# Optimization experiments

Measured on AMD Instinct MI355X. Metric: run time of the kernel, lower is better.

## Reference

```python
import jax, jax.numpy as jnp
import numpy as np

B, N, E = 4, 160, 200000
D_EDGE, D_ORI, D_TYPE = 128, 8, 120      # d_edge, d_ori_edge, d_edge_type = d_edge - d_ori_edge
D_EXT = 512                               # d_edge * expansion_factor(4)
D_H4 = 512                                # d_edge * 4
D_REL = 16
PML, ETN = 32, 16                         # path_max_length, edge_type_num


def setup_inputs() -> dict:
    key = jax.random.key(0)
    ks = jax.random.split(key, 16)
    p = lambda i, shape, s=0.05: (jax.random.normal(ks[i], shape) * s).astype(jnp.float32)
    return dict(
        rel_type=jax.random.randint(ks[0], (E,), 0, ETN),
        rel_error=jax.random.normal(ks[1], (E, D_ORI), jnp.float32),
        edge_pos=jax.random.randint(ks[2], (E,), 0, PML),
        dist=jax.random.randint(ks[3], (B, N, N), 0, PML),
        rel_row=jnp.sort(jax.random.randint(ks[4], (E,), 0, B * N * N)),
        rel_col=jax.random.randint(ks[5], (E,), 0, 10000),
        batch_num=B, max_node=N,
        type_tab=p(6, (ETN, D_TYPE), 1.0),
        pos_tab=p(7, (PML, D_EDGE), 1.0),
        dist_tab=p(8, (PML, D_EXT), 1.0),
        w1=p(9, (D_EDGE, 2 * D_EDGE)), b1=jnp.zeros(2 * D_EDGE, jnp.float32),
        w2=p(10, (2 * D_EDGE, 4 * D_EDGE)), b2=jnp.zeros(4 * D_EDGE, jnp.float32),
        w3=p(11, (4 * D_EDGE, D_EXT)), b3=jnp.zeros(D_EXT, jnp.float32),
        g1=jnp.ones(D_EXT, jnp.float32), be1=jnp.zeros(D_EXT, jnp.float32),
        wf1=p(12, (D_EXT, D_H4)), bf1=jnp.zeros(D_H4, jnp.float32),
        g2=jnp.ones(D_H4, jnp.float32), be2=jnp.zeros(D_H4, jnp.float32),
        wf2=p(13, (D_H4, D_H4)), bf2=jnp.zeros(D_H4, jnp.float32),
        g3=jnp.ones(D_H4, jnp.float32), be3=jnp.zeros(D_H4, jnp.float32),
        wf3=p(14, (D_H4, D_REL)), bf3=jnp.zeros(D_REL, jnp.float32),
    )


def _ln(x, g, b, eps=1e-5):
    m = x.mean(-1, keepdims=True)
    v = ((x - m) ** 2).mean(-1, keepdims=True)
    return (x - m) * jax.lax.rsqrt(v + eps) * g + b


def reference(rel_type, rel_error, edge_pos, dist, rel_row, rel_col, batch_num, max_node,
              type_tab, pos_tab, dist_tab,
              w1, b1, w2, b2, w3, b3,
              g1, be1, wf1, bf1, g2, be2, wf2, bf2, g3, be3, wf3, bf3):
    type_tab = type_tab.at[0].set(0.0)   # padding_idx=0
    dist_tab = dist_tab.at[0].set(0.0)   # padding_idx=0
    # embed + concat + positional add  -> [E, D_EDGE]
    e = jnp.concatenate([type_tab[rel_type], rel_error], axis=1) + pos_tab[edge_pos]
    # point-net style edge MLP -> [E, D_EXT]
    h = jax.nn.relu(e @ w1 + b1)
    h = jax.nn.relu(h @ w2 + b2)
    h = h @ w3 + b3
    # sparse scatter-max over the hybrid-COO row index (torch_sparse.reduce.max, dim=1)
    n_seg = batch_num * max_node * max_node
    seg = jax.ops.segment_max(h, rel_row, num_segments=n_seg, indices_are_sorted=True)
    seg = jnp.where(jnp.isneginf(seg), 0.0, seg)   # empty rows -> 0 (torch_scatter fill)
    rel = seg.reshape(batch_num, max_node, max_node, -1) + dist_tab[dist]
    # fc: ReLU, LN, Linear, ReLU, LN, Linear, ReLU, LN, Linear
    x = _ln(jax.nn.relu(rel), g1, be1) @ wf1 + bf1
    x = _ln(jax.nn.relu(x), g2, be2) @ wf2 + bf2
    x = _ln(jax.nn.relu(x), g3, be3) @ wf3 + bf3   # [B, N, N, D_REL]
    # triu over the (N, N) dims, then symmetrize
    mask = jnp.triu(jnp.ones((max_node, max_node), x.dtype))
    x = x * mask[None, :, :, None]
    return x + x.transpose(0, 2, 1, 3)
```

## Files before the change

kernel.cpp:

```cpp
#include <hip/hip_runtime.h>

typedef __attribute__((ext_vector_type(8))) _Float16 half8;
typedef __attribute__((ext_vector_type(4))) _Float16 half4;
typedef __attribute__((ext_vector_type(4))) float f32x4;

constexpr int Bn = 4;
constexpr int Nn = 160;
constexpr int SEGN = Bn * Nn * Nn;
constexpr int TRIN = Nn * (Nn + 1) / 2;
constexpr int CMPN = Bn * TRIN;
constexpr int SCAN_NB = (SEGN + 511) / 512;

__device__ __forceinline__ int tri_base(int i) { return i * Nn - (i * (i - 1)) / 2; }

__global__ void k_prep(const float* __restrict__ w1, const float* __restrict__ w2,
                       const float* __restrict__ w3, const float* __restrict__ wf1,
                       const float* __restrict__ wf2, const float* __restrict__ wf3,
                       _Float16* __restrict__ o1, _Float16* __restrict__ o2,
                       _Float16* __restrict__ o3, _Float16* __restrict__ of1,
                       _Float16* __restrict__ of2, _Float16* __restrict__ of3) {
  int t = blockIdx.x * 256 + threadIdx.x;
  const float* src; _Float16* dst; int N, local; bool is3 = false;
  if (t < 32768)       { src = w1;  dst = o1;  N = 256; local = t; }
  else if (t < 163840) { src = w2;  dst = o2;  N = 512; local = t - 32768; }
  else if (t < 425984) { src = w3;  dst = o3;  N = 512; local = t - 163840; }
  else if (t < 688128) { src = wf1; dst = of1; N = 512; local = t - 425984; }
  else if (t < 950272) { src = wf2; dst = of2; N = 512; local = t - 688128; }
  else if (t < 958464) { src = wf3; dst = of3; N = 16;  local = t - 950272; is3 = true; }
  else return;
  int k = local / N;
  int n = local - k * N;
  if (is3) dst[n * 512 + k] = (_Float16)src[local];
  else dst[(size_t)((k >> 5) * N + n) * 32 + (k & 31)] = (_Float16)src[local];
}

__device__ __forceinline__ int lower_bound_rr(const int* __restrict__ rel_row, int E, int key) {
  int lo = 0, hi = E;
  while (lo < hi) { int mid = (lo + hi) >> 1; if (rel_row[mid] < key) lo = mid + 1; else hi = mid; }
  return lo;
}

__global__ void k_cnt(const int* __restrict__ rel_row, int* __restrict__ row_ptr,
                      int* __restrict__ cnt, int* __restrict__ tri2ij, int E) {
  int r = blockIdx.x * 256 + threadIdx.x;
  if (r < TRIN) {
    int lo = 0, hi = Nn - 1;
    while (lo < hi) { int mid = (lo + hi + 1) >> 1; if (tri_base(mid) <= r) lo = mid; else hi = mid - 1; }
    int j = lo + (r - tri_base(lo));
    tri2ij[r] = (lo << 16) | j;
  }
  if (r > SEGN) return;
  int lo = lower_bound_rr(rel_row, E, r);
  row_ptr[r] = lo;
  if (r < SEGN) {
    int hi2 = lower_bound_rr(rel_row, E, r + 1);
    int jj = r % Nn;
    int ii = (r / Nn) % Nn;
    cnt[r] = (ii <= jj) ? (hi2 - lo) : 0;
  }
}

__global__ void k_scan1(const int* __restrict__ cnt, int* __restrict__ pre,
                        int* __restrict__ bsum) {
  __shared__ int tmp[512];
  int t = threadIdx.x, b = blockIdx.x;
  int idx = b * 512 + t;
  int v = (idx < SEGN) ? cnt[idx] : 0;
  tmp[t] = v;
  __syncthreads();
  for (int o = 1; o < 512; o <<= 1) {
    int add = (t >= o) ? tmp[t - o] : 0;
    __syncthreads();
    tmp[t] += add;
    __syncthreads();
  }
  if (idx < SEGN) pre[idx] = tmp[t] - v;
  if (t == 511) bsum[b] = tmp[511];
}

__global__ void k_scan2(int* __restrict__ bsum, int* __restrict__ ek) {
  __shared__ int tmp[256];
  int t = threadIdx.x;
  int v = (t < SCAN_NB) ? bsum[t] : 0;
  tmp[t] = v;
  __syncthreads();
  for (int o = 1; o < 256; o <<= 1) {
    int add = (t >= o) ? tmp[t - o] : 0;
    __syncthreads();
    tmp[t] += add;
    __syncthreads();
  }
  if (t < SCAN_NB) bsum[t] = tmp[t] - v;
  if (t == 255) ek[0] = tmp[255];
}

__global__ void k_map(const int* __restrict__ row_ptr, const int* __restrict__ cnt,
                      const int* __restrict__ pre, const int* __restrict__ bsum,
                      int* __restrict__ cstart, int* __restrict__ edge_map) {
  int r = blockIdx.x * 512 + threadIdx.x;
  if (r >= SEGN) return;
  int cs = pre[r] + bsum[r >> 9];
  cstart[r] = cs;
  int c = cnt[r];
  int rp = row_ptr[r];
  for (int k = 0; k < c; ++k) edge_map[cs + k] = rp + k;
  if (r == SEGN - 1) cstart[SEGN] = cs + c;
}

template <int MT, int K, int C0, int CN, int NSTRIDE, int NT, bool SP>
__device__ __forceinline__ void do_slice(const _Float16* __restrict__ wt,
                                         const char* a_base, int nbase,
                                         f32x4 (&acc)[MT][NT], int tid) {
  constexpr int rowB = K * 2;
  const int w = tid >> 6, lane = tid & 63, ln15 = lane & 15, kg = lane >> 4;
  const char* wb = (const char*)wt;
#pragma unroll
  for (int c = 0; c < CN; ++c) {
    half8 a[MT], b[NT];
#pragma unroll
    for (int nt = 0; nt < NT; ++nt) {
      int n = nbase + (w * NT + nt) * 16 + ln15;
      b[nt] = *(const half8*)(wb + (size_t)(C0 + c) * (NSTRIDE * 64) + n * 64 + kg * 16);
    }
#pragma unroll
    for (int mt = 0; mt < MT; ++mt) {
      int row = mt * 16 + ln15;
      int byte = (row * rowB + c * 64 + kg * 16) ^ ((row & 7) << 4);
      a[mt] = *(const half8*)(a_base + byte);
    }
    if (SP) __builtin_amdgcn_s_setprio(1);
#pragma unroll
    for (int mt = 0; mt < MT; ++mt)
#pragma unroll
      for (int nt = 0; nt < NT; ++nt)
        acc[mt][nt] = __builtin_amdgcn_mfma_f32_16x16x32_f16(a[mt], b[nt], acc[mt][nt], 0, 0, 0);
    if (SP) __builtin_amdgcn_s_setprio(0);
  }
}

template <int MT, int NT>
__device__ __forceinline__ void init_accn(const float* __restrict__ bias, int nbase,
                                          f32x4 (&acc)[MT][NT], int tid) {
  const int w = tid >> 6, ln15 = tid & 15;
#pragma unroll
  for (int nt = 0; nt < NT; ++nt) {
    float bv = bias[nbase + (w * NT + nt) * 16 + ln15];
    f32x4 s = {bv, bv, bv, bv};
#pragma unroll
    for (int mt = 0; mt < MT; ++mt) acc[mt][nt] = s;
  }
}

template <int MT, int NT, bool RELU>
__device__ __forceinline__ void store_hn(char* h, int rowB, int nbase,
                                         const f32x4 (&acc)[MT][NT], int tid) {
  const int w = tid >> 6, lane = tid & 63, ln15 = lane & 15, kg = lane >> 4;
#pragma unroll
  for (int mt = 0; mt < MT; ++mt)
#pragma unroll
    for (int nt = 0; nt < NT; ++nt)
#pragma unroll
      for (int j = 0; j < 4; ++j) {
        int row = mt * 16 + kg * 4 + j;
        int n = nbase + (w * NT + nt) * 16 + ln15;
        float v = acc[mt][nt][j];
        if (RELU) v = fmaxf(v, 0.f);
        *(_Float16*)(h + ((row * rowB + n * 2) ^ ((row & 7) << 4))) = (_Float16)v;
      }
}

__global__ __launch_bounds__(512) void k_edge(
    const int* __restrict__ rel_type, const float* __restrict__ rel_error,
    const int* __restrict__ edge_pos, const int* __restrict__ edge_map,
    const int* __restrict__ ekp,
    const float* __restrict__ type_tab, const float* __restrict__ pos_tab,
    const _Float16* __restrict__ w1t, const float* __restrict__ b1,
    const _Float16* __restrict__ w2t, const float* __restrict__ b2,
    const _Float16* __restrict__ w3t, const float* __restrict__ b3,
    _Float16* __restrict__ h3) {
  __shared__ __align__(16) char smem[98304];
  char* h1 = smem;
  char* h2 = smem + 32768;
  char* e  = smem + 32768;

  const int tid = threadIdx.x;
  const int e0 = blockIdx.x * 64;
  const int EK = ekp[0];
  if (e0 >= EK) return;

  {
    int r = tid >> 3, c0 = (tid & 7) * 16;
    int re = edge_map[min(e0 + r, EK - 1)];
    int rt = rel_type[re];
    int ep = edge_pos[re];
#pragma unroll
    for (int s = 0; s < 2; ++s) {
      half8 hv;
#pragma unroll
      for (int q = 0; q < 8; ++q) {
        int cc = c0 + s * 8 + q;
        float v = (cc < 120) ? (rt ? type_tab[rt * 120 + cc] : 0.f)
                             : rel_error[(size_t)re * 8 + (cc - 120)];
        v += pos_tab[ep * 128 + cc];
        hv[q] = (_Float16)v;
      }
      int byte = (r * 256 + (c0 + s * 8) * 2) ^ ((r & 7) << 4);
      *(half8*)(e + byte) = hv;
    }
  }
  __syncthreads();

  {
    f32x4 acc[4][2];
    init_accn<4, 2>(b1, 0, acc, tid);
    do_slice<4, 128, 0, 4, 256, 2, true>(w1t, e, 0, acc, tid);
    store_hn<4, 2, true>(h1, 512, 0, acc, tid);
  }
  __syncthreads();
  {
    f32x4 acc[4][4];
    init_accn<4, 4>(b2, 0, acc, tid);
    do_slice<4, 256, 0, 8, 512, 4, true>(w2t, h1, 0, acc, tid);
    store_hn<4, 4, true>(h2, 1024, 0, acc, tid);
  }
  __syncthreads();
  {
    f32x4 acc[4][4];
    init_accn<4, 4>(b3, 0, acc, tid);
    do_slice<4, 512, 0, 16, 512, 4, true>(w3t, h2, 0, acc, tid);
    __syncthreads();
    store_hn<4, 4, false>(h2, 1024, 0, acc, tid);
    __syncthreads();
    uint4* dst = (uint4*)(h3 + (size_t)e0 * 512);
#pragma unroll
    for (int i = 0; i < 8; ++i) {
      int cidx = tid + i * 512;
      int byteoff = cidx * 16;
      int row = byteoff >> 10;
      uint4 v = *(const uint4*)(h2 + (byteoff ^ ((row & 7) << 4)));
      if (e0 + row < EK) dst[cidx] = v;
    }
  }
}

__global__ __launch_bounds__(256) void k_gather(
    const _Float16* __restrict__ h3, const int* __restrict__ cstart,
    const int* __restrict__ tri2ij, const int* __restrict__ dist,
    const float* __restrict__ dist_tab,
    const float* __restrict__ g1, const float* __restrict__ be1,
    _Float16* __restrict__ rowsA) {
  const int w = threadIdx.x >> 6, lane = threadIdx.x & 63;
  const int coff = lane * 8;
  const float* gp = g1 + coff;
  const float* bp = be1 + coff;
  const _Float16 NEGH = (_Float16)(-65504.f);
  const int pbase = blockIdx.x * 32 + w * 8;
  for (int rr = 0; rr < 8; ++rr) {
    int p = pbase + rr;
    if (p >= CMPN) return;
    int b = p / TRIN;
    int ij = tri2ij[p - b * TRIN];
    int gr = (b * Nn + (ij >> 16)) * Nn + (ij & 0xffff);
    int s = cstart[gr], en = cstart[gr + 1];
    int di = dist[gr];
    half8 mx;
#pragma unroll
    for (int q = 0; q < 8; ++q) mx[q] = NEGH;
    int idx = s;
    while (idx + 4 <= en) {
      half8 c0 = *(const half8*)(h3 + (size_t)(idx + 0) * 512 + coff);
      half8 c1 = *(const half8*)(h3 + (size_t)(idx + 1) * 512 + coff);
      half8 c2 = *(const half8*)(h3 + (size_t)(idx + 2) * 512 + coff);
      half8 c3 = *(const half8*)(h3 + (size_t)(idx + 3) * 512 + coff);
      mx = __builtin_elementwise_max(mx, __builtin_elementwise_max(
               __builtin_elementwise_max(c0, c1), __builtin_elementwise_max(c2, c3)));
      idx += 4;
    }
    if (idx + 2 <= en) {
      half8 c0 = *(const half8*)(h3 + (size_t)(idx + 0) * 512 + coff);
      half8 c1 = *(const half8*)(h3 + (size_t)(idx + 1) * 512 + coff);
      mx = __builtin_elementwise_max(mx, __builtin_elementwise_max(c0, c1));
      idx += 2;
    }
    if (idx < en) {
      half8 c0 = *(const half8*)(h3 + (size_t)idx * 512 + coff);
      mx = __builtin_elementwise_max(mx, c0);
    }
    const float* dt = dist_tab + (size_t)di * 512 + coff;
    float v[8]; float s1 = 0.f, s2 = 0.f;
#pragma unroll
    for (int q = 0; q < 8; ++q) {
      float vv = (s == en) ? 0.f : (float)mx[q];
      if (di) vv += dt[q];
      vv = fmaxf(vv, 0.f);
      v[q] = vv; s1 += vv; s2 += vv * vv;
    }
#pragma unroll
    for (int o = 32; o > 0; o >>= 1) { s1 += __shfl_xor(s1, o); s2 += __shfl_xor(s2, o); }
    float mean = s1 * (1.f / 512.f);
    float rs = rsqrtf(s2 * (1.f / 512.f) - mean * mean + 1e-5f);
    half8 ov;
#pragma unroll
    for (int q = 0; q < 8; ++q) ov[q] = (_Float16)((v[q] - mean) * rs * gp[q] + bp[q]);
    *(half8*)((char*)rowsA + (size_t)p * 1024 + ((coff * 2) ^ ((p & 7) << 4))) = ov;
  }
}

__device__ __forceinline__ void epi_ln_store(f32x4 (&acc)[4][4], char* dst,
                                             float* st1, float* st2,
                                             float* stM, float* stR,
                                             const float* __restrict__ g,
                                             const float* __restrict__ be, int tid) {
  const int w = tid >> 6, lane = tid & 63, ln15 = lane & 15, kg = lane >> 4;
#pragma unroll
  for (int mt = 0; mt < 4; ++mt)
#pragma unroll
    for (int nt = 0; nt < 4; ++nt)
#pragma unroll
      for (int j = 0; j < 4; ++j) acc[mt][nt][j] = fmaxf(acc[mt][nt][j], 0.f);
#pragma unroll
  for (int mt = 0; mt < 4; ++mt)
#pragma unroll
    for (int j = 0; j < 4; ++j) {
      float a = 0.f, b = 0.f;
#pragma unroll
      for (int nt = 0; nt < 4; ++nt) { float v = acc[mt][nt][j]; a += v; b += v * v; }
#pragma unroll
      for (int m = 1; m < 16; m <<= 1) { a += __shfl_xor(a, m); b += __shfl_xor(b, m); }
      if (ln15 == 0) {
        int r = mt * 16 + kg * 4 + j;
        st1[w * 64 + r] = a;
        st2[w * 64 + r] = b;
      }
    }
  __syncthreads();
  if (tid < 64) {
    float a = 0.f, b = 0.f;
#pragma unroll
    for (int ww = 0; ww < 8; ++ww) { a += st1[ww * 64 + tid]; b += st2[ww * 64 + tid]; }
    float mean = a * (1.f / 512.f);
    float var = b * (1.f / 512.f) - mean * mean;
    stM[tid] = mean;
    stR[tid] = rsqrtf(var + 1e-5f);
  }
  __syncthreads();
  float gv[4], bv[4];
#pragma unroll
  for (int nt = 0; nt < 4; ++nt) {
    int n = (w * 4 + nt) * 16 + ln15;
    gv[nt] = g[n]; bv[nt] = be[n];
  }
#pragma unroll
  for (int mt = 0; mt < 4; ++mt)
#pragma unroll
    for (int j = 0; j < 4; ++j) {
      int r = mt * 16 + kg * 4 + j;
      float mean = stM[r], rs = stR[r];
#pragma unroll
      for (int nt = 0; nt < 4; ++nt) {
        int n = (w * 4 + nt) * 16 + ln15;
        float v = (acc[mt][nt][j] - mean) * rs * gv[nt] + bv[nt];
        *(_Float16*)(dst + ((r * 1024 + n * 2) ^ ((r & 7) << 4))) = (_Float16)v;
      }
    }
  __syncthreads();
}

__global__ __launch_bounds__(512, 2) void k_fcg(
    const _Float16* __restrict__ rowsA,
    const float* __restrict__ g2, const float* __restrict__ be2,
    const _Float16* __restrict__ wf1t, const float* __restrict__ bf1,
    const float* __restrict__ g3, const float* __restrict__ be3,
    const _Float16* __restrict__ wf2t, const float* __restrict__ bf2,
    const _Float16* __restrict__ wf3t, const float* __restrict__ bf3,
    float* __restrict__ x3c) {
  __shared__ __align__(16) char bufA[65536];
  __shared__ float st1[512], st2[512];
  __shared__ float stM[64], stR[64];

  const int tid = threadIdx.x;
  const int p0 = blockIdx.x * 64;

  {
    const uint4* src = (const uint4*)((const char*)rowsA + (size_t)p0 * 1024);
    uint4* dst = (uint4*)bufA;
#pragma unroll
    for (int i = 0; i < 8; ++i) dst[tid + i * 512] = src[tid + i * 512];
  }
  __syncthreads();

  {
    f32x4 acc[4][4];
    init_accn<4, 4>(bf1, 0, acc, tid);
    do_slice<4, 512, 0, 16, 512, 4, true>(wf1t, bufA, 0, acc, tid);
    epi_ln_store(acc, bufA, st1, st2, stM, stR, g2, be2, tid);
  }
  {
    f32x4 acc[4][4];
    init_accn<4, 4>(bf2, 0, acc, tid);
    do_slice<4, 512, 0, 16, 512, 4, true>(wf2t, bufA, 0, acc, tid);
    epi_ln_store(acc, bufA, st1, st2, stM, stR, g3, be3, tid);
  }
  {
    const int w = tid >> 6, lane = tid & 63, ln15 = lane & 15, kg = lane >> 4;
    if (w < 4) {
      f32x4 acc3 = {0.f, 0.f, 0.f, 0.f};
#pragma unroll
      for (int c = 0; c < 16; ++c) {
        half8 b = *(const half8*)((const char*)wf3t + ln15 * 1024 + c * 64 + kg * 16);
        int row = w * 16 + ln15;
        half8 a = *(const half8*)(bufA + ((row * 1024 + c * 64 + kg * 16) ^ ((row & 7) << 4)));
        acc3 = __builtin_amdgcn_mfma_f32_16x16x32_f16(a, b, acc3, 0, 0, 0);
      }
#pragma unroll
      for (int j = 0; j < 4; ++j)
        x3c[(size_t)(p0 + w * 16 + kg * 4 + j) * 16 + ln15] = acc3[j] + bf3[ln15];
    }
  }
}

__global__ void k_sym(const float* __restrict__ x3c, float* __restrict__ out) {
  int t = blockIdx.x * 256 + threadIdx.x;
  if (t >= SEGN * 4) return;
  int q = t & 3;
  int cell = t >> 2;
  int j = cell % Nn;
  int tmp = cell / Nn;
  int i = tmp % Nn;
  int b = tmp / Nn;
  int lo = min(i, j), hi = i ^ j ^ lo;
  int p = b * TRIN + tri_base(lo) + (hi - lo);
  float4 v = *(const float4*)&x3c[(size_t)p * 16 + q * 4];
  if (i == j) { v.x *= 2.f; v.y *= 2.f; v.z *= 2.f; v.w *= 2.f; }
  *(float4*)&out[(size_t)t * 4] = v;
}

extern "C" void kernel_launch(void* const* d_in, const int* in_sizes, int n_in,
                              void* d_out, int out_size, void* d_ws, size_t ws_size,
                              hipStream_t stream) {
  const int*   rel_type  = (const int*)d_in[0];
  const float* rel_error = (const float*)d_in[1];
  const int*   edge_pos  = (const int*)d_in[2];
  const int*   dist      = (const int*)d_in[3];
  const int*   rel_row   = (const int*)d_in[4];
  const float* type_tab = (const float*)d_in[8];
  const float* pos_tab  = (const float*)d_in[9];
  const float* dist_tab = (const float*)d_in[10];
  const float* w1 = (const float*)d_in[11]; const float* b1 = (const float*)d_in[12];
  const float* w2 = (const float*)d_in[13]; const float* b2 = (const float*)d_in[14];
  const float* w3 = (const float*)d_in[15]; const float* b3 = (const float*)d_in[16];
  const float* g1 = (const float*)d_in[17]; const float* be1 = (const float*)d_in[18];
  const float* wf1 = (const float*)d_in[19]; const float* bf1 = (const float*)d_in[20];
  const float* g2 = (const float*)d_in[21]; const float* be2 = (const float*)d_in[22];
  const float* wf2 = (const float*)d_in[23]; const float* bf2 = (const float*)d_in[24];
  const float* g3 = (const float*)d_in[25]; const float* be3 = (const float*)d_in[26];
  const float* wf3 = (const float*)d_in[27]; const float* bf3 = (const float*)d_in[28];

  const int E = in_sizes[0];
  const size_t h3_bytes   = (size_t)E * 512 * 2;
  const size_t rows_off   = ((size_t)E * 55 / 100) * 1024;
  const size_t x3_bytes   = (size_t)CMPN * 16 * 4;
  const size_t ptr_bytes  = (size_t)(SEGN + 1) * 4;
  const size_t tri_bytes  = (size_t)TRIN * 4;
  const size_t cell_bytes = (size_t)SEGN * 4;
  const size_t cst_bytes  = (size_t)(SEGN + 1) * 4;
  const size_t map_bytes  = (size_t)E * 4;
  const size_t wt_elems   = 32768 + 131072 + 262144 * 3 + 8192;
  const size_t total = h3_bytes + x3_bytes + ptr_bytes + tri_bytes + 2 * cell_bytes +
                       cst_bytes + map_bytes + 1024 + 256 * 4 + wt_elems * 2;
  if (ws_size < total) return;

  char* wp = (char*)d_ws;
  _Float16* h3      = (_Float16*)wp;
  _Float16* rowsA   = (_Float16*)(wp + rows_off);
  wp += h3_bytes;
  float*    x3c     = (float*)wp;               wp += x3_bytes;
  int*      row_ptr = (int*)wp;                 wp += ptr_bytes;
  int*      tri2ij  = (int*)wp;                 wp += tri_bytes;
  int*      cnt     = (int*)wp;                 wp += cell_bytes;
  int*      pre     = (int*)wp;                 wp += cell_bytes;
  int*      cstart  = (int*)wp;                 wp += cst_bytes;
  int*      edge_map= (int*)wp;                 wp += map_bytes;
  int*      bsum    = (int*)wp;                 wp += 256 * 4;
  int*      ekp     = (int*)wp;                 wp += 1024;
  _Float16* w1t     = (_Float16*)wp;
  _Float16* w2t  = w1t + 32768;
  _Float16* w3t  = w2t + 131072;
  _Float16* wf1t = w3t + 262144;
  _Float16* wf2t = wf1t + 262144;
  _Float16* wf3t = wf2t + 262144;
  float*    out  = (float*)d_out;

  k_prep<<<3744, 256, 0, stream>>>(w1, w2, w3, wf1, wf2, wf3,
                                   w1t, w2t, w3t, wf1t, wf2t, wf3t);
  k_cnt<<<(SEGN + 256) / 256, 256, 0, stream>>>(rel_row, row_ptr, cnt, tri2ij, E);
  k_scan1<<<SCAN_NB, 512, 0, stream>>>(cnt, pre, bsum);
  k_scan2<<<1, 256, 0, stream>>>(bsum, ekp);
  k_map<<<SCAN_NB, 512, 0, stream>>>(row_ptr, cnt, pre, bsum, cstart, edge_map);
  k_edge<<<(E + 63) / 64, 512, 0, stream>>>(rel_type, rel_error, edge_pos, edge_map, ekp,
                                            type_tab, pos_tab, w1t, b1, w2t, b2, w3t, b3,
                                            h3);
  k_gather<<<(CMPN + 31) / 32, 256, 0, stream>>>(h3, cstart, tri2ij, dist, dist_tab,
                                                 g1, be1, rowsA);
  k_fcg<<<CMPN / 64, 512, 0, stream>>>(rowsA,
                                       g2, be2, wf1t, bf1,
                                       g3, be3, wf2t, bf2,
                                       wf3t, bf3, x3c);
  k_sym<<<(SEGN * 4 + 255) / 256, 256, 0, stream>>>(x3c, out);
}
```

Baseline: 375.4 us.

## Stage edge-MLP weights through LDS with async double-buffered global_load_lds

```diff
diff --git a/kernel.cpp b/kernel.cpp
--- a/kernel.cpp
+++ b/kernel.cpp
@@ -12,6 +12,12 @@
 constexpr int SCAN_NB = (SEGN + 511) / 512;
 
 __device__ __forceinline__ int tri_base(int i) { return i * Nn - (i * (i - 1)) / 2; }
+
+__device__ __forceinline__ void gload_lds16(const void* g, void* l) {
+  __builtin_amdgcn_global_load_lds(
+      (const __attribute__((address_space(1))) unsigned int*)g,
+      (__attribute__((address_space(3))) unsigned int*)l, 16, 0, 0);
+}
 
 __global__ void k_prep(const float* __restrict__ w1, const float* __restrict__ w2,
                        const float* __restrict__ w3, const float* __restrict__ wf1,
@@ -20,18 +26,23 @@
                        _Float16* __restrict__ o3, _Float16* __restrict__ of1,
                        _Float16* __restrict__ of2, _Float16* __restrict__ of3) {
   int t = blockIdx.x * 256 + threadIdx.x;
-  const float* src; _Float16* dst; int N, local; bool is3 = false;
+  const float* src; _Float16* dst; int N, local; int mode = 0;
   if (t < 32768)       { src = w1;  dst = o1;  N = 256; local = t; }
   else if (t < 163840) { src = w2;  dst = o2;  N = 512; local = t - 32768; }
   else if (t < 425984) { src = w3;  dst = o3;  N = 512; local = t - 163840; }
-  else if (t < 688128) { src = wf1; dst = of1; N = 512; local = t - 425984; }
-  else if (t < 950272) { src = wf2; dst = of2; N = 512; local = t - 688128; }
-  else if (t < 958464) { src = wf3; dst = of3; N = 16;  local = t - 950272; is3 = true; }
+  else if (t < 688128) { src = wf1; dst = of1; N = 512; local = t - 425984; mode = 1; }
+  else if (t < 950272) { src = wf2; dst = of2; N = 512; local = t - 688128; mode = 1; }
+  else if (t < 958464) { src = wf3; dst = of3; N = 16;  local = t - 950272; mode = 2; }
   else return;
   int k = local / N;
   int n = local - k * N;
-  if (is3) dst[n * 512 + k] = (_Float16)src[local];
-  else dst[(size_t)((k >> 5) * N + n) * 32 + (k & 31)] = (_Float16)src[local];
+  if (mode == 2) dst[n * 512 + k] = (_Float16)src[local];
+  else if (mode == 1)
+    dst[(size_t)((k >> 5) * N + n) * 32 + (k & 31)] = (_Float16)src[local];
+  else {
+    int s = ((k >> 3) & 3) ^ ((n >> 1) & 3);
+    dst[(size_t)(k >> 5) * (N * 32) + n * 32 + (s << 3) + (k & 7)] = (_Float16)src[local];
+  }
 }
 
 __device__ __forceinline__ int lower_bound_rr(const int* __restrict__ rel_row, int E, int key) {
@@ -138,6 +149,56 @@
   }
 }
 
+template <int K, int NT>
+__device__ __forceinline__ void do_layer_st(const _Float16* __restrict__ wt,
+                                            const char* a_base, char* wb0, char* wb1,
+                                            f32x4 (&acc)[4][NT], int tid) {
+  constexpr int C = K / 32;
+  constexpr int N = NT * 128;
+  constexpr int CB = N * 64;
+  constexpr int U = CB / 8192;
+  constexpr int rowB = K * 2;
+  const int w = tid >> 6, lane = tid & 63, ln15 = lane & 15, kg = lane >> 4;
+  const char* src = (const char*)wt;
+
+#pragma unroll
+  for (int u = 0; u < U; ++u)
+    gload_lds16(src + u * 8192 + tid * 16, wb0 + u * 8192 + tid * 16);
+  __syncthreads();
+
+#pragma unroll
+  for (int c = 0; c < C; ++c) {
+    char* cur = (c & 1) ? wb1 : wb0;
+    char* nxt = (c & 1) ? wb0 : wb1;
+    if (c + 1 < C) {
+#pragma unroll
+      for (int u = 0; u < U; ++u)
+        gload_lds16(src + (size_t)(c + 1) * CB + u * 8192 + tid * 16,
+                    nxt + u * 8192 + tid * 16);
+    }
+    half8 a[4], b[NT];
+#pragma unroll
+    for (int nt = 0; nt < NT; ++nt) {
+      int n = (w * NT + nt) * 16 + ln15;
+      b[nt] = *(const half8*)(cur + n * 64 + ((kg ^ ((n >> 1) & 3)) << 4));
+    }
+#pragma unroll
+    for (int mt = 0; mt < 4; ++mt) {
+      int row = mt * 16 + ln15;
+      int byte = (row * rowB + c * 64 + kg * 16) ^ ((row & 7) << 4);
+      a[mt] = *(const half8*)(a_base + byte);
+    }
+    __builtin_amdgcn_s_setprio(1);
+#pragma unroll
+    for (int mt = 0; mt < 4; ++mt)
+#pragma unroll
+      for (int nt = 0; nt < NT; ++nt)
+        acc[mt][nt] = __builtin_amdgcn_mfma_f32_16x16x32_f16(a[mt], b[nt], acc[mt][nt], 0, 0, 0);
+    __builtin_amdgcn_s_setprio(0);
+    __syncthreads();
+  }
+}
+
 template <int MT, int NT>
 __device__ __forceinline__ void init_accn(const float* __restrict__ bias, int nbase,
                                           f32x4 (&acc)[MT][NT], int tid) {
@@ -178,10 +239,13 @@
     const _Float16* __restrict__ w2t, const float* __restrict__ b2,
     const _Float16* __restrict__ w3t, const float* __restrict__ b3,
     _Float16* __restrict__ h3) {
-  __shared__ __align__(16) char smem[98304];
-  char* h1 = smem;
-  char* h2 = smem + 32768;
-  char* e  = smem + 32768;
+  __shared__ __align__(16) char smem[131072];
+  char* hbuf = smem;
+  char* wb0  = smem + 65536;
+  char* wb1  = smem + 98304;
+  char* e  = hbuf;
+  char* h1 = hbuf + 32768;
+  char* h2 = hbuf;
 
   const int tid = threadIdx.x;
   const int e0 = blockIdx.x * 64;
@@ -213,22 +277,21 @@
   {
     f32x4 acc[4][2];
     init_accn<4, 2>(b1, 0, acc, tid);
-    do_slice<4, 128, 0, 4, 256, 2, true>(w1t, e, 0, acc, tid);
+    do_layer_st<128, 2>(w1t, e, wb0, wb1, acc, tid);
     store_hn<4, 2, true>(h1, 512, 0, acc, tid);
   }
   __syncthreads();
-  {
-    f32x4 acc[4][4];
-    init_accn<4, 4>(b2, 0, acc, tid);
-    do_slice<4, 256, 0, 8, 512, 4, true>(w2t, h1, 0, acc, tid);
-    store_hn<4, 4, true>(h2, 1024, 0, acc, tid);
+  f32x4 acc2[4][4];
+  {
+    init_accn<4, 4>(b2, 0, acc2, tid);
+    do_layer_st<256, 4>(w2t, h1, wb0, wb1, acc2, tid);
+    store_hn<4, 4, true>(h2, 1024, 0, acc2, tid);
   }
   __syncthreads();
   {
     f32x4 acc[4][4];
     init_accn<4, 4>(b3, 0, acc, tid);
-    do_slice<4, 512, 0, 16, 512, 4, true>(w3t, h2, 0, acc, tid);
-    __syncthreads();
+    do_layer_st<512, 4>(w3t, h2, wb0, wb1, acc, tid);
     store_hn<4, 4, false>(h2, 1024, 0, acc, tid);
     __syncthreads();
     uint4* dst = (uint4*)(h3 + (size_t)e0 * 512);
```

New measurement: 387.3 us. 1.03x slower.
